# Kernel tuning notes

Measured on AMD Instinct MI355X. Metric: run time of the kernel, lower is better.

The kernel has to match this reference:

```python
import jax, jax.numpy as jnp
import numpy as np

# dims
B, SL, RATIO = 2, 2048, 16
SG = SL // RATIO            # 128 global tokens
S = SL + SG                 # 2176 combined sequence
V, D, H, F, L, NC = 32000, 512, 8, 2048, 2, 8
HD = D // H
PAD = 0


def setup_inputs() -> dict:
    key = jax.random.key(0)
    ks = iter(jax.random.split(key, 40))
    def n(shape, s=0.02):
        return jax.random.normal(next(ks), shape, dtype=jnp.float32) * s
    token_ids = jax.random.randint(next(ks), (B, SL), 0, V)
    embed_table = n((V, D), 1.0).at[PAD].set(0.0)  # padding_idx row is zero
    return {
        "token_ids": token_ids,
        "embed_table": embed_table,
        "global_embed": n((D,), 1.0),              # shared learned global token
        "in_proj_w": n((L, 3 * D, D)), "in_proj_b": jnp.zeros((L, 3 * D)),
        "out_w": n((L, D, D)), "out_b": jnp.zeros((L, D)),
        "ln1_g": jnp.ones((L, D)), "ln1_b": jnp.zeros((L, D)),
        "ln2_g": jnp.ones((L, D)), "ln2_b": jnp.zeros((L, D)),
        "ff1_w": n((L, F, D)), "ff1_b": jnp.zeros((L, F)),
        "ff2_w": n((L, D, F)), "ff2_b": jnp.zeros((L, D)),
        "cls_w1": n((D // 2, D)), "cls_w2": n((NC, D // 2)),
    }


def _layernorm(x, g, b, eps=1e-5):
    mu = x.mean(-1, keepdims=True)
    var = ((x - mu) ** 2).mean(-1, keepdims=True)
    return (x - mu) * jax.lax.rsqrt(var + eps) * g + b


def _etc_bias(pad_long, pad_glob):
    # structured local/global mask: l2l block-diagonal by segment, l2g/g2l
    # long<->its own global token, g2g full. All four components enabled.
    seg = jnp.repeat(jnp.arange(SG), RATIO)          # (SL,) segment id per long token
    gid = jnp.arange(SG)
    l2l = seg[:, None] == seg[None, :]               # (SL, SL)
    l2g = seg[:, None] == gid[None, :]               # (SL, SG)
    allowed = jnp.block([[l2l, l2g],
                         [l2g.T, jnp.ones((SG, SG), bool)]])  # (S, S)
    kpad = jnp.concatenate([pad_long, pad_glob], axis=1)       # (B, S)
    ok = allowed[None] & (~kpad)[:, None, :]
    return jnp.where(ok, 0.0, -1e9)[:, None]          # (B, 1, S, S)


def reference(token_ids, embed_table, global_embed, in_proj_w, in_proj_b,
              out_w, out_b, ln1_g, ln1_b, ln2_g, ln2_b,
              ff1_w, ff1_b, ff2_w, ff2_b, cls_w1, cls_w2):
    pad_long = token_ids == PAD                      # (B, SL)
    pad_glob = pad_long.reshape(B, SG, RATIO).all(-1)  # (B, SG)
    x_long = embed_table[token_ids]                  # (B, SL, D)
    x_glob = jnp.broadcast_to(global_embed, (B, SG, D))
    x = jnp.concatenate([x_long, x_glob], axis=1)    # (B, S, D)
    bias = _etc_bias(pad_long, pad_glob)
    scale = 1.0 / np.sqrt(HD)
    for i in range(L):  # post-norm TransformerEncoderLayer, relu FFN, dropout=0
        qkv = x @ in_proj_w[i].T + in_proj_b[i]
        q, k, v = jnp.split(qkv, 3, axis=-1)
        q = q.reshape(B, S, H, HD)
        k = k.reshape(B, S, H, HD)
        v = v.reshape(B, S, H, HD)
        att = jnp.einsum('bqhd,bkhd->bhqk', q, k) * scale + bias
        att = jax.nn.softmax(att, axis=-1)
        o = jnp.einsum('bhqk,bkhd->bqhd', att, v).reshape(B, S, D)
        x = _layernorm(x + o @ out_w[i].T + out_b[i], ln1_g[i], ln1_b[i])
        h = jax.nn.relu(x @ ff1_w[i].T + ff1_b[i])
        x = _layernorm(x + h @ ff2_w[i].T + ff2_b[i], ln2_g[i], ln2_b[i])
    # masked mean-pool over global tokens
    zg = jnp.where(pad_glob[..., None], 0.0, x[:, SL:, :])
    denom = (~pad_glob).sum(axis=1, keepdims=True).astype(zg.dtype)
    z_cls = zg.sum(axis=1) / denom                   # (B, D)
    return jax.nn.relu(z_cls @ cls_w1.T) @ cls_w2.T  # (B, NC)
```

## Files before the change

### kernel.cpp

```cpp
#include <hip/hip_runtime.h>
#include <hip/hip_bf16.h>
#include <stdint.h>


namespace {

constexpr int kB  = 2;
constexpr int kSL = 2048;
constexpr int kSG = 128;
constexpr int kS  = 2176;
constexpr int kD  = 512;
constexpr int kH  = 8;
constexpr int kF  = 2048;
constexpr int kNC = 8;
constexpr int kM  = kB * kS;

typedef __bf16 bf16x8 __attribute__((ext_vector_type(8)));
typedef unsigned short u16x8 __attribute__((ext_vector_type(8)));
typedef float  f32x4  __attribute__((ext_vector_type(4)));
using bf16 = __hip_bfloat16;

__device__ __forceinline__ void gload16(const void* g, void* l) {
  __builtin_amdgcn_global_load_lds(
      (const __attribute__((address_space(1))) void*)g,
      (__attribute__((address_space(3))) void*)l, 16, 0, 0);
}

__device__ __forceinline__ float bfu2f(unsigned short u) {
  return __uint_as_float(((unsigned int)u) << 16);
}

__global__ __launch_bounds__(256) void cvt4_kernel(
    const float* __restrict__ s0, bf16* __restrict__ d0,
    const float* __restrict__ s1, bf16* __restrict__ d1,
    const float* __restrict__ s2, bf16* __restrict__ d2,
    const float* __restrict__ s3, bf16* __restrict__ d3) {
  constexpr int n0 = 2 * 1536 * 512 / 4;
  constexpr int n1 = 2 * 512 * 512 / 4;
  constexpr int n2 = 2 * 2048 * 512 / 4;
  constexpr int n3 = 2 * 512 * 2048 / 4;
  constexpr int total = n0 + n1 + n2 + n3;
  for (int i = blockIdx.x * 256 + threadIdx.x; i < total;
       i += gridDim.x * 256) {
    const float* src;
    bf16* dst;
    int j = i;
    if (j < n0) { src = s0; dst = d0; }
    else if ((j -= n0) < n1) { src = s1; dst = d1; }
    else if ((j -= n1) < n2) { src = s2; dst = d2; }
    else { j -= n2; src = s3; dst = d3; }
    float4 v = ((const float4*)src)[j];
    dst[j * 4 + 0] = __float2bfloat16(v.x);
    dst[j * 4 + 1] = __float2bfloat16(v.y);
    dst[j * 4 + 2] = __float2bfloat16(v.z);
    dst[j * 4 + 3] = __float2bfloat16(v.w);
  }
}

__global__ __launch_bounds__(128) void embed_kernel(
    const int* __restrict__ tok, const float* __restrict__ table,
    const float* __restrict__ gemb, float* __restrict__ x,
    bf16* __restrict__ x_bf, unsigned char* __restrict__ pad_long) {
  const int row = blockIdx.x;
  const int b = row / kS, s = row % kS;
  const int t = threadIdx.x;
  const float* src;
  if (s < kSL) {
    const int tk = tok[b * kSL + s];
    if (t == 0) pad_long[b * kSL + s] = (tk == 0) ? 1 : 0;
    src = table + (size_t)tk * kD;
  } else {
    src = gemb;
  }
  float4 v = *(const float4*)(src + t * 4);
  *(float4*)(x + (size_t)row * kD + t * 4) = v;
  bf16* xb = x_bf + (size_t)row * kD + t * 4;
  xb[0] = __float2bfloat16(v.x);
  xb[1] = __float2bfloat16(v.y);
  xb[2] = __float2bfloat16(v.z);
  xb[3] = __float2bfloat16(v.w);
}

__global__ void pad_glob_kernel(const int* __restrict__ tok,
                                unsigned char* __restrict__ pad_glob) {
  const int i = threadIdx.x;
  if (i < kB * kSG) {
    const int b = i >> 7, g = i & 127;
    bool all = true;
    for (int j = 0; j < 16; ++j) all = all && (tok[b * kSL + g * 16 + j] == 0);
    pad_glob[i] = all ? 1 : 0;
  }
}

template <int OUT_MODE>
__global__ __launch_bounds__(256) void gemm_bt(
    const bf16* __restrict__ A, const bf16* __restrict__ W,
    const float* __restrict__ bias, void* __restrict__ Cout,
    int M, int N, int K) {
  __shared__ __align__(16) bf16 As[128 * 32];
  __shared__ __align__(16) bf16 Bs[128 * 32];
  const int t = threadIdx.x;
  const int lane = t & 63;
  const int wid = t >> 6;
  const int wm = wid >> 1, wn = wid & 1;
  const int bm = blockIdx.y * 128, bn = blockIdx.x * 128;
  const int srow = t >> 2, scol = (t & 3) * 8;

  f32x4 acc[4][4];
#pragma unroll
  for (int mi = 0; mi < 4; ++mi)
#pragma unroll
    for (int ni = 0; ni < 4; ++ni)
#pragma unroll
      for (int r = 0; r < 4; ++r) acc[mi][ni][r] = 0.f;

  const bf16* a0 = A + (size_t)(bm + srow) * K + scol;
  const bf16* a1 = a0 + (size_t)64 * K;
  const bf16* w0 = W + (size_t)(bn + srow) * K + scol;
  const bf16* w1p = w0 + (size_t)64 * K;

  for (int k0 = 0; k0 < K; k0 += 32) {
    gload16(a0 + k0, &As[t * 8]);
    gload16(a1 + k0, &As[2048 + t * 8]);
    gload16(w0 + k0, &Bs[t * 8]);
    gload16(w1p + k0, &Bs[2048 + t * 8]);
    __syncthreads();
    bf16x8 af[4], wf[4];
#pragma unroll
    for (int mi = 0; mi < 4; ++mi)
      af[mi] = *(const bf16x8*)&As[(wm * 64 + mi * 16 + (lane & 15)) * 32 +
                                   (lane >> 4) * 8];
#pragma unroll
    for (int ni = 0; ni < 4; ++ni)
      wf[ni] = *(const bf16x8*)&Bs[(wn * 64 + ni * 16 + (lane & 15)) * 32 +
                                   (lane >> 4) * 8];
#pragma unroll
    for (int mi = 0; mi < 4; ++mi)
#pragma unroll
      for (int ni = 0; ni < 4; ++ni)
        acc[mi][ni] = __builtin_amdgcn_mfma_f32_16x16x32_bf16(
            af[mi], wf[ni], acc[mi][ni], 0, 0, 0);
    __syncthreads();
  }

  const int lr = (lane >> 4) * 4;
  const int lc = lane & 15;
#pragma unroll
  for (int ni = 0; ni < 4; ++ni) {
    const int col = bn + wn * 64 + ni * 16 + lc;
    const float bv = bias ? bias[col] : 0.f;
#pragma unroll
    for (int mi = 0; mi < 4; ++mi) {
#pragma unroll
      for (int r = 0; r < 4; ++r) {
        const int row = bm + wm * 64 + mi * 16 + lr + r;
        float v = acc[mi][ni][r] + bv;
        if (OUT_MODE == 2) v = fmaxf(v, 0.f);
        if (OUT_MODE == 0)
          ((float*)Cout)[(size_t)row * N + col] = v;
        else
          ((bf16*)Cout)[(size_t)row * N + col] = __float2bfloat16(v);
      }
    }
  }
}

template <int OUT_MODE>
__global__ __launch_bounds__(256) void gemm_bt_64(
    const bf16* __restrict__ A, const bf16* __restrict__ W,
    const float* __restrict__ bias, void* __restrict__ Cout,
    int M, int N, int K) {
  __shared__ __align__(16) bf16 As[64 * 32];
  __shared__ __align__(16) bf16 Bs[64 * 32];
  const int t = threadIdx.x;
  const int lane = t & 63;
  const int wid = t >> 6;
  const int wm = wid >> 1, wn = wid & 1;
  const int bm = blockIdx.y * 64, bn = blockIdx.x * 64;
  const int srow = t >> 2, scol = (t & 3) * 8;

  f32x4 acc[2][2];
#pragma unroll
  for (int mi = 0; mi < 2; ++mi)
#pragma unroll
    for (int ni = 0; ni < 2; ++ni)
#pragma unroll
      for (int r = 0; r < 4; ++r) acc[mi][ni][r] = 0.f;

  const bf16* a0 = A + (size_t)(bm + srow) * K + scol;
  const bf16* w0 = W + (size_t)(bn + srow) * K + scol;

  for (int k0 = 0; k0 < K; k0 += 32) {
    gload16(a0 + k0, &As[t * 8]);
    gload16(w0 + k0, &Bs[t * 8]);
    __syncthreads();
    bf16x8 af[2], wf[2];
#pragma unroll
    for (int mi = 0; mi < 2; ++mi)
      af[mi] = *(const bf16x8*)&As[(wm * 32 + mi * 16 + (lane & 15)) * 32 +
                                   (lane >> 4) * 8];
#pragma unroll
    for (int ni = 0; ni < 2; ++ni)
      wf[ni] = *(const bf16x8*)&Bs[(wn * 32 + ni * 16 + (lane & 15)) * 32 +
                                   (lane >> 4) * 8];
#pragma unroll
    for (int mi = 0; mi < 2; ++mi)
#pragma unroll
      for (int ni = 0; ni < 2; ++ni)
        acc[mi][ni] = __builtin_amdgcn_mfma_f32_16x16x32_bf16(
            af[mi], wf[ni], acc[mi][ni], 0, 0, 0);
    __syncthreads();
  }

  const int lr = (lane >> 4) * 4;
  const int lc = lane & 15;
#pragma unroll
  for (int ni = 0; ni < 2; ++ni) {
    const int col = bn + wn * 32 + ni * 16 + lc;
    const float bv = bias ? bias[col] : 0.f;
#pragma unroll
    for (int mi = 0; mi < 2; ++mi) {
#pragma unroll
      for (int r = 0; r < 4; ++r) {
        const int row = bm + wm * 32 + mi * 16 + lr + r;
        float v = acc[mi][ni][r] + bv;
        if (OUT_MODE == 2) v = fmaxf(v, 0.f);
        if (OUT_MODE == 0)
          ((float*)Cout)[(size_t)row * N + col] = v;
        else
          ((bf16*)Cout)[(size_t)row * N + col] = __float2bfloat16(v);
      }
    }
  }
}

__global__ __launch_bounds__(64) void attn_kernel(
    const bf16* __restrict__ qkv, const unsigned char* __restrict__ padl,
    const unsigned char* __restrict__ padg, bf16* __restrict__ o) {
  __shared__ float lds_buf[17 * 64 * 2];
  const int blk0 = blockIdx.x;
  const int g = blk0 & 127;
  const int h = (blk0 >> 7) & 7;
  const int b = (blk0 >> 10) & 1;
  const int t = threadIdx.x;

  if (blk0 < 2048) {
    float* Ks = lds_buf;
    float* Vs = lds_buf + 17 * 64;
    const int qi = t >> 2, part = t & 3;
    for (int e = t; e < 17 * 64; e += 64) {
      const int j = e >> 6, d = e & 63;
      const size_t row = (j < 16) ? (size_t)(b * kS + g * 16 + j)
                                  : (size_t)(b * kS + kSL + g);
      const bf16* base = qkv + row * (3 * kD) + h * 64 + d;
      Ks[e] = __bfloat162float(base[512]);
      Vs[e] = __bfloat162float(base[1024]);
    }
    __syncthreads();

    float qv[16];
    {
      const bf16* qb = qkv + (size_t)(b * kS + g * 16 + qi) * (3 * kD) +
                       h * 64 + part * 16;
#pragma unroll
      for (int d = 0; d < 16; ++d) qv[d] = __bfloat162float(qb[d]);
    }
    float sc[17];
#pragma unroll
    for (int j = 0; j < 17; ++j) {
      float s = 0.f;
      const float* kb = &Ks[j * 64 + part * 16];
#pragma unroll
      for (int d = 0; d < 16; ++d) s += qv[d] * kb[d];
      s += __shfl_xor(s, 1);
      s += __shfl_xor(s, 2);
      const bool pad = (j < 16) ? (padl[b * kSL + g * 16 + j] != 0)
                                : (padg[b * kSG + g] != 0);
      sc[j] = s * 0.125f + (pad ? -1e9f : 0.f);
    }
    float m = sc[0];
#pragma unroll
    for (int j = 1; j < 17; ++j) m = fmaxf(m, sc[j]);
    float l = 0.f;
#pragma unroll
    for (int j = 0; j < 17; ++j) {
      sc[j] = __expf(sc[j] - m);
      l += sc[j];
    }
    const float inv = 1.f / l;
    float ov[16];
#pragma unroll
    for (int d = 0; d < 16; ++d) ov[d] = 0.f;
#pragma unroll
    for (int j = 0; j < 17; ++j) {
      const float* vb = &Vs[j * 64 + part * 16];
#pragma unroll
      for (int d = 0; d < 16; ++d) ov[d] += sc[j] * vb[d];
    }
    bf16* ob = o + (size_t)(b * kS + g * 16 + qi) * kD + h * 64 + part * 16;
#pragma unroll
    for (int d = 0; d < 16; ++d) ob[d] = __float2bfloat16(ov[d] * inv);
  } else {
    float* q_lds = lds_buf;
    float* p_lds = lds_buf + 64;
    const size_t qrow = (size_t)(b * kS + kSL + g);
    const unsigned short* qkv_u = (const unsigned short*)qkv;
    q_lds[t] = bfu2f(qkv_u[qrow * 1536 + h * 64 + t]);
    __syncthreads();

    float sc[3];
#pragma unroll
    for (int c = 0; c < 3; ++c) {
      const int j = t + c * 64;
      float s = -3.0e38f;
      if (j < 144) {
        const size_t krow = (j < 16) ? (size_t)(b * kS + g * 16 + j)
                                     : (size_t)(b * kS + kSL + (j - 16));
        const u16x8* kb = (const u16x8*)(qkv_u + krow * 1536 + 512 + h * 64);
        float acc = 0.f;
#pragma unroll
        for (int d0 = 0; d0 < 8; ++d0) {
          u16x8 kv = kb[d0];
#pragma unroll
          for (int u = 0; u < 8; ++u) acc += q_lds[d0 * 8 + u] * bfu2f(kv[u]);
        }
        const bool pad = (j < 16) ? (padl[b * kSL + g * 16 + j] != 0)
                                  : (padg[b * kSG + (j - 16)] != 0);
        s = acc * 0.125f + (pad ? -1e9f : 0.f);
      }
      sc[c] = s;
    }
    float m = fmaxf(fmaxf(sc[0], sc[1]), sc[2]);
#pragma unroll
    for (int off = 1; off < 64; off <<= 1) m = fmaxf(m, __shfl_xor(m, off));
    float lsum = 0.f;
#pragma unroll
    for (int c = 0; c < 3; ++c) {
      const int j = t + c * 64;
      if (j < 144) {
        const float p = __expf(sc[c] - m);
        p_lds[j] = p;
        lsum += p;
      }
    }
#pragma unroll
    for (int off = 1; off < 64; off <<= 1) lsum += __shfl_xor(lsum, off);
    __syncthreads();
    const float inv = 1.f / lsum;

    float ov = 0.f;
#pragma unroll 8
    for (int j = 0; j < 144; ++j) {
      const size_t vrow = (j < 16) ? (size_t)(b * kS + g * 16 + j)
                                   : (size_t)(b * kS + kSL + (j - 16));
      ov += p_lds[j] * bfu2f(qkv_u[vrow * 1536 + 1024 + h * 64 + t]);
    }
    o[qrow * kD + h * 64 + t] = __float2bfloat16(ov * inv);
  }
}

__global__ __launch_bounds__(256) void residual_ln_kernel(
    float* __restrict__ x, const float* __restrict__ tmp,
    const float* __restrict__ gamma, const float* __restrict__ beta,
    bf16* __restrict__ x_bf) {
  const int row = blockIdx.x, t = threadIdx.x;
  const size_t base = (size_t)row * kD;
  float v0 = x[base + t] + tmp[base + t];
  float v1 = x[base + t + 256] + tmp[base + t + 256];
  float s = v0 + v1, q = v0 * v0 + v1 * v1;
#pragma unroll
  for (int off = 32; off > 0; off >>= 1) {
    s += __shfl_down(s, off);
    q += __shfl_down(q, off);
  }
  __shared__ float rs[4], rq[4];
  const int wid = t >> 6;
  if ((t & 63) == 0) { rs[wid] = s; rq[wid] = q; }
  __syncthreads();
  const float S = rs[0] + rs[1] + rs[2] + rs[3];
  const float Q = rq[0] + rq[1] + rq[2] + rq[3];
  const float mean = S * (1.f / kD);
  const float var = Q * (1.f / kD) - mean * mean;
  const float inv = rsqrtf(var + 1e-5f);
  const float y0 = (v0 - mean) * inv * gamma[t] + beta[t];
  const float y1 = (v1 - mean) * inv * gamma[t + 256] + beta[t + 256];
  x[base + t] = y0;
  x[base + t + 256] = y1;
  x_bf[base + t] = __float2bfloat16(y0);
  x_bf[base + t + 256] = __float2bfloat16(y1);
}

__global__ __launch_bounds__(256) void pool_kernel(
    const float* __restrict__ x, const unsigned char* __restrict__ padg,
    float* __restrict__ z) {
  const int b = blockIdx.x >> 5;
  const int d0 = (blockIdx.x & 31) * 16;
  const int gg = threadIdx.x >> 4, dl = threadIdx.x & 15;
  float acc = 0.f;
  int cnt = 0;
#pragma unroll
  for (int k = 0; k < 8; ++k) {
    const int g = k * 16 + gg;
    if (padg[b * kSG + g] == 0) {
      acc += x[(size_t)(b * kS + kSL + g) * kD + d0 + dl];
      ++cnt;
    }
  }
  __shared__ float red[256];
  __shared__ int redc[256];
  red[threadIdx.x] = acc;
  redc[threadIdx.x] = cnt;
  __syncthreads();
  for (int s = 8; s > 0; s >>= 1) {
    if (gg < s) {
      red[gg * 16 + dl] += red[(gg + s) * 16 + dl];
      redc[gg * 16 + dl] += redc[(gg + s) * 16 + dl];
    }
    __syncthreads();
  }
  if (gg == 0) z[b * kD + d0 + dl] = red[dl] / (float)redc[dl];
}

__global__ __launch_bounds__(256) void cls1_kernel(
    const float* __restrict__ z, const float* __restrict__ w1,
    float* __restrict__ h1) {
  const int wv = (blockIdx.x * 256 + threadIdx.x) >> 6;
  const int lane = threadIdx.x & 63;
  const int b = wv >> 8, t = wv & 255;
  const float4* zp = (const float4*)(z + b * kD);
  const float4* wp = (const float4*)(w1 + (size_t)t * kD);
  float4 a0 = zp[lane * 2], a1 = zp[lane * 2 + 1];
  float4 b0 = wp[lane * 2], b1 = wp[lane * 2 + 1];
  float acc = a0.x * b0.x + a0.y * b0.y + a0.z * b0.z + a0.w * b0.w +
              a1.x * b1.x + a1.y * b1.y + a1.z * b1.z + a1.w * b1.w;
#pragma unroll
  for (int off = 32; off > 0; off >>= 1) acc += __shfl_down(acc, off);
  if (lane == 0) h1[wv] = fmaxf(acc, 0.f);
}

__global__ __launch_bounds__(64) void cls2_kernel(
    const float* __restrict__ h1, const float* __restrict__ w2,
    float* __restrict__ out) {
  const int wv = blockIdx.x;
  const int lane = threadIdx.x;
  const int b = wv >> 3, c = wv & 7;
  float4 h4 = ((const float4*)(h1 + b * 256))[lane];
  float4 w4 = ((const float4*)(w2 + c * 256))[lane];
  float acc = h4.x * w4.x + h4.y * w4.y + h4.z * w4.z + h4.w * w4.w;
#pragma unroll
  for (int off = 32; off > 0; off >>= 1) acc += __shfl_down(acc, off);
  if (lane == 0) out[wv] = acc;
}

}

extern "C" void kernel_launch(void* const* d_in, const int* in_sizes, int n_in,
                              void* d_out, int out_size, void* d_ws,
                              size_t ws_size, hipStream_t stream) {
  (void)in_sizes; (void)n_in; (void)out_size; (void)ws_size;
  const int*   token_ids    = (const int*)d_in[0];
  const float* embed_table  = (const float*)d_in[1];
  const float* global_embed = (const float*)d_in[2];
  const float* in_proj_w    = (const float*)d_in[3];
  const float* in_proj_b    = (const float*)d_in[4];
  const float* out_w        = (const float*)d_in[5];
  const float* out_b        = (const float*)d_in[6];
  const float* ln1_g        = (const float*)d_in[7];
  const float* ln1_b        = (const float*)d_in[8];
  const float* ln2_g        = (const float*)d_in[9];
  const float* ln2_b        = (const float*)d_in[10];
  const float* ff1_w        = (const float*)d_in[11];
  const float* ff1_b        = (const float*)d_in[12];
  const float* ff2_w        = (const float*)d_in[13];
  const float* ff2_b        = (const float*)d_in[14];
  const float* cls_w1       = (const float*)d_in[15];
  const float* cls_w2       = (const float*)d_in[16];
  float* out = (float*)d_out;

  char* ws = (char*)d_ws;
  size_t off = 0;
  auto alloc = [&](size_t bytes) -> void* {
    void* p = ws + off;
    off += (bytes + 255) & ~(size_t)255;
    return p;
  };
  float* x_f   = (float*)alloc((size_t)kM * kD * 4);
  bf16*  x_b   = (bf16*)alloc((size_t)kM * kD * 2);
  bf16*  qkv_b = (bf16*)alloc((size_t)kM * 3 * kD * 2);
  bf16*  o_b   = (bf16*)alloc((size_t)kM * kD * 2);
  float* tmp_f = (float*)alloc((size_t)kM * kD * 4);
  bf16*  h_b   = (bf16*)alloc((size_t)kM * kF * 2);
  bf16*  wqkv  = (bf16*)alloc((size_t)2 * 1536 * 512 * 2);
  bf16*  wout  = (bf16*)alloc((size_t)2 * 512 * 512 * 2);
  bf16*  wff1  = (bf16*)alloc((size_t)2 * 2048 * 512 * 2);
  bf16*  wff2  = (bf16*)alloc((size_t)2 * 512 * 2048 * 2);
  unsigned char* padl = (unsigned char*)alloc(kB * kSL);
  unsigned char* padg = (unsigned char*)alloc(kB * kSG);
  float* z_f   = (float*)alloc((size_t)kB * kD * 4);
  float* h1_f  = (float*)alloc((size_t)kB * 256 * 4);

  cvt4_kernel<<<2048, 256, 0, stream>>>(in_proj_w, wqkv, out_w, wout,
                                        ff1_w, wff1, ff2_w, wff2);

  embed_kernel<<<kM, 128, 0, stream>>>(token_ids, embed_table, global_embed,
                                       x_f, x_b, padl);
  pad_glob_kernel<<<1, 256, 0, stream>>>(token_ids, padg);

  for (int l = 0; l < 2; ++l) {
    gemm_bt<1><<<dim3(1536 / 128, kM / 128), 256, 0, stream>>>(
        x_b, wqkv + (size_t)l * 1536 * 512, in_proj_b + l * 1536, qkv_b,
        kM, 1536, 512);
    attn_kernel<<<2 * kB * kH * kSG, 64, 0, stream>>>(qkv_b, padl, padg, o_b);
    gemm_bt_64<0><<<dim3(512 / 64, kM / 64), 256, 0, stream>>>(
        o_b, wout + (size_t)l * 512 * 512, out_b + l * 512, tmp_f,
        kM, 512, 512);
    residual_ln_kernel<<<kM, 256, 0, stream>>>(x_f, tmp_f, ln1_g + l * 512,
                                               ln1_b + l * 512, x_b);
    gemm_bt<2><<<dim3(2048 / 128, kM / 128), 256, 0, stream>>>(
        x_b, wff1 + (size_t)l * 2048 * 512, ff1_b + l * 2048, h_b,
        kM, 2048, 512);
    gemm_bt_64<0><<<dim3(512 / 64, kM / 64), 256, 0, stream>>>(
        h_b, wff2 + (size_t)l * 512 * 2048, ff2_b + l * 512, tmp_f,
        kM, 512, 2048);
    residual_ln_kernel<<<kM, 256, 0, stream>>>(x_f, tmp_f, ln2_g + l * 512,
                                               ln2_b + l * 512, x_b);
  }

  pool_kernel<<<kB * 32, 256, 0, stream>>>(x_f, padg, z_f);
  cls1_kernel<<<128, 256, 0, stream>>>(z_f, cls_w1, h1_f);
  cls2_kernel<<<16, 64, 0, stream>>>(h1_f, cls_w2, out);
}
```

Before: 373.3 us.

## Fuse residual add into N=512 GEMM epilogue and fold pad_glob into embed

```diff
diff --git a/kernel.cpp b/kernel.cpp
--- a/kernel.cpp
+++ b/kernel.cpp
@@ -60,10 +60,21 @@
 __global__ __launch_bounds__(128) void embed_kernel(
     const int* __restrict__ tok, const float* __restrict__ table,
     const float* __restrict__ gemb, float* __restrict__ x,
-    bf16* __restrict__ x_bf, unsigned char* __restrict__ pad_long) {
+    bf16* __restrict__ x_bf, unsigned char* __restrict__ pad_long,
+    unsigned char* __restrict__ pad_glob) {
   const int row = blockIdx.x;
+  const int t = threadIdx.x;
+  if (row == kM) {
+    for (int i = t; i < kB * kSG; i += 128) {
+      const int b = i >> 7, g = i & 127;
+      bool all = true;
+      for (int j = 0; j < 16; ++j)
+        all = all && (tok[b * kSL + g * 16 + j] == 0);
+      pad_glob[i] = all ? 1 : 0;
+    }
+    return;
+  }
   const int b = row / kS, s = row % kS;
-  const int t = threadIdx.x;
   const float* src;
   if (s < kSL) {
     const int tk = tok[b * kSL + s];
@@ -79,17 +90,6 @@
   xb[1] = __float2bfloat16(v.y);
   xb[2] = __float2bfloat16(v.z);
   xb[3] = __float2bfloat16(v.w);
-}
-
-__global__ void pad_glob_kernel(const int* __restrict__ tok,
-                                unsigned char* __restrict__ pad_glob) {
-  const int i = threadIdx.x;
-  if (i < kB * kSG) {
-    const int b = i >> 7, g = i & 127;
-    bool all = true;
-    for (int j = 0; j < 16; ++j) all = all && (tok[b * kSL + g * 16 + j] == 0);
-    pad_glob[i] = all ? 1 : 0;
-  }
 }
 
 template <int OUT_MODE>
@@ -148,7 +148,7 @@
 #pragma unroll
   for (int ni = 0; ni < 4; ++ni) {
     const int col = bn + wn * 64 + ni * 16 + lc;
-    const float bv = bias ? bias[col] : 0.f;
+    const float bv = bias[col];
 #pragma unroll
     for (int mi = 0; mi < 4; ++mi) {
 #pragma unroll
@@ -156,55 +156,52 @@
         const int row = bm + wm * 64 + mi * 16 + lr + r;
         float v = acc[mi][ni][r] + bv;
         if (OUT_MODE == 2) v = fmaxf(v, 0.f);
-        if (OUT_MODE == 0)
-          ((float*)Cout)[(size_t)row * N + col] = v;
-        else
-          ((bf16*)Cout)[(size_t)row * N + col] = __float2bfloat16(v);
+        ((bf16*)Cout)[(size_t)row * N + col] = __float2bfloat16(v);
       }
     }
   }
 }
 
-template <int OUT_MODE>
-__global__ __launch_bounds__(256) void gemm_bt_64(
+__global__ __launch_bounds__(256) void gemm_res(
     const bf16* __restrict__ A, const bf16* __restrict__ W,
-    const float* __restrict__ bias, void* __restrict__ Cout,
-    int M, int N, int K) {
-  __shared__ __align__(16) bf16 As[64 * 32];
+    const float* __restrict__ bias, float* __restrict__ X, int K) {
+  __shared__ __align__(16) bf16 As[128 * 32];
   __shared__ __align__(16) bf16 Bs[64 * 32];
   const int t = threadIdx.x;
   const int lane = t & 63;
   const int wid = t >> 6;
   const int wm = wid >> 1, wn = wid & 1;
-  const int bm = blockIdx.y * 64, bn = blockIdx.x * 64;
+  const int bm = blockIdx.y * 128, bn = blockIdx.x * 64;
   const int srow = t >> 2, scol = (t & 3) * 8;
 
-  f32x4 acc[2][2];
-#pragma unroll
-  for (int mi = 0; mi < 2; ++mi)
+  f32x4 acc[4][2];
+#pragma unroll
+  for (int mi = 0; mi < 4; ++mi)
 #pragma unroll
     for (int ni = 0; ni < 2; ++ni)
 #pragma unroll
       for (int r = 0; r < 4; ++r) acc[mi][ni][r] = 0.f;
 
   const bf16* a0 = A + (size_t)(bm + srow) * K + scol;
+  const bf16* a1 = a0 + (size_t)64 * K;
   const bf16* w0 = W + (size_t)(bn + srow) * K + scol;
 
   for (int k0 = 0; k0 < K; k0 += 32) {
     gload16(a0 + k0, &As[t * 8]);
+    gload16(a1 + k0, &As[2048 + t * 8]);
     gload16(w0 + k0, &Bs[t * 8]);
     __syncthreads();
-    bf16x8 af[2], wf[2];
-#pragma unroll
-    for (int mi = 0; mi < 2; ++mi)
-      af[mi] = *(const bf16x8*)&As[(wm * 32 + mi * 16 + (lane & 15)) * 32 +
+    bf16x8 af[4], wf[2];
+#pragma unroll
+    for (int mi = 0; mi < 4; ++mi)
+      af[mi] = *(const bf16x8*)&As[(wm * 64 + mi * 16 + (lane & 15)) * 32 +
                                    (lane >> 4) * 8];
 #pragma unroll
     for (int ni = 0; ni < 2; ++ni)
       wf[ni] = *(const bf16x8*)&Bs[(wn * 32 + ni * 16 + (lane & 15)) * 32 +
                                    (lane >> 4) * 8];
 #pragma unroll
-    for (int mi = 0; mi < 2; ++mi)
+    for (int mi = 0; mi < 4; ++mi)
 #pragma unroll
       for (int ni = 0; ni < 2; ++ni)
         acc[mi][ni] = __builtin_amdgcn_mfma_f32_16x16x32_bf16(
@@ -217,18 +214,14 @@
 #pragma unroll
   for (int ni = 0; ni < 2; ++ni) {
     const int col = bn + wn * 32 + ni * 16 + lc;
-    const float bv = bias ? bias[col] : 0.f;
-#pragma unroll
-    for (int mi = 0; mi < 2; ++mi) {
+    const float bv = bias[col];
+#pragma unroll
+    for (int mi = 0; mi < 4; ++mi) {
 #pragma unroll
       for (int r = 0; r < 4; ++r) {
-        const int row = bm + wm * 32 + mi * 16 + lr + r;
-        float v = acc[mi][ni][r] + bv;
-        if (OUT_MODE == 2) v = fmaxf(v, 0.f);
-        if (OUT_MODE == 0)
-          ((float*)Cout)[(size_t)row * N + col] = v;
-        else
-          ((bf16*)Cout)[(size_t)row * N + col] = __float2bfloat16(v);
+        const int row = bm + wm * 64 + mi * 16 + lr + r;
+        float* xp = X + (size_t)row * kD + col;
+        *xp = *xp + acc[mi][ni][r] + bv;
       }
     }
   }
@@ -359,14 +352,13 @@
   }
 }
 
-__global__ __launch_bounds__(256) void residual_ln_kernel(
-    float* __restrict__ x, const float* __restrict__ tmp,
-    const float* __restrict__ gamma, const float* __restrict__ beta,
-    bf16* __restrict__ x_bf) {
+__global__ __launch_bounds__(256) void ln_kernel(
+    float* __restrict__ x, const float* __restrict__ gamma,
+    const float* __restrict__ beta, bf16* __restrict__ x_bf) {
   const int row = blockIdx.x, t = threadIdx.x;
   const size_t base = (size_t)row * kD;
-  float v0 = x[base + t] + tmp[base + t];
-  float v1 = x[base + t + 256] + tmp[base + t + 256];
+  float v0 = x[base + t];
+  float v1 = x[base + t + 256];
   float s = v0 + v1, q = v0 * v0 + v1 * v1;
 #pragma unroll
   for (int off = 32; off > 0; off >>= 1) {
@@ -488,7 +480,6 @@
   bf16*  x_b   = (bf16*)alloc((size_t)kM * kD * 2);
   bf16*  qkv_b = (bf16*)alloc((size_t)kM * 3 * kD * 2);
   bf16*  o_b   = (bf16*)alloc((size_t)kM * kD * 2);
-  float* tmp_f = (float*)alloc((size_t)kM * kD * 4);
   bf16*  h_b   = (bf16*)alloc((size_t)kM * kF * 2);
   bf16*  wqkv  = (bf16*)alloc((size_t)2 * 1536 * 512 * 2);
   bf16*  wout  = (bf16*)alloc((size_t)2 * 512 * 512 * 2);
@@ -502,28 +493,25 @@
   cvt4_kernel<<<2048, 256, 0, stream>>>(in_proj_w, wqkv, out_w, wout,
                                         ff1_w, wff1, ff2_w, wff2);
 
-  embed_kernel<<<kM, 128, 0, stream>>>(token_ids, embed_table, global_embed,
-                                       x_f, x_b, padl);
-  pad_glob_kernel<<<1, 256, 0, stream>>>(token_ids, padg);
+  embed_kernel<<<kM + 1, 128, 0, stream>>>(token_ids, embed_table,
+                                           global_embed, x_f, x_b, padl, padg);
 
   for (int l = 0; l < 2; ++l) {
     gemm_bt<1><<<dim3(1536 / 128, kM / 128), 256, 0, stream>>>(
         x_b, wqkv + (size_t)l * 1536 * 512, in_proj_b + l * 1536, qkv_b,
         kM, 1536, 512);
     attn_kernel<<<2 * kB * kH * kSG, 64, 0, stream>>>(qkv_b, padl, padg, o_b);
-    gemm_bt_64<0><<<dim3(512 / 64, kM / 64), 256, 0, stream>>>(
-        o_b, wout + (size_t)l * 512 * 512, out_b + l * 512, tmp_f,
-        kM, 512, 512);
-    residual_ln_kernel<<<kM, 256, 0, stream>>>(x_f, tmp_f, ln1_g + l * 512,
-                                               ln1_b + l * 512, x_b);
+    gemm_res<<<dim3(512 / 64, kM / 128), 256, 0, stream>>>(
+        o_b, wout + (size_t)l * 512 * 512, out_b + l * 512, x_f, 512);
+    ln_kernel<<<kM, 256, 0, stream>>>(x_f, ln1_g + l * 512, ln1_b + l * 512,
+                                      x_b);
     gemm_bt<2><<<dim3(2048 / 128, kM / 128), 256, 0, stream>>>(
         x_b, wff1 + (size_t)l * 2048 * 512, ff1_b + l * 2048, h_b,
         kM, 2048, 512);
-    gemm_bt_64<0><<<dim3(512 / 64, kM / 64), 256, 0, stream>>>(
-        h_b, wff2 + (size_t)l * 512 * 2048, ff2_b + l * 512, tmp_f,
-        kM, 512, 2048);
-    residual_ln_kernel<<<kM, 256, 0, stream>>>(x_f, tmp_f, ln2_g + l * 512,
-                                               ln2_b + l * 512, x_b);
+    gemm_res<<<dim3(512 / 64, kM / 128), 256, 0, stream>>>(
+        h_b, wff2 + (size_t)l * 512 * 2048, ff2_b + l * 512, x_f, 2048);
+    ln_kernel<<<kM, 256, 0, stream>>>(x_f, ln2_g + l * 512, ln2_b + l * 512,
+                                      x_b);
   }
 
   pool_kernel<<<kB * 32, 256, 0, stream>>>(x_f, padg, z_f);
```

New measurement: 397.0 us. +6.4%, slower.
